# Performance work log

Hardware: AMD Instinct MI355X
Metric: run time of the kernel (lower is better)

## Reference

```python
import jax, jax.numpy as jnp
import numpy as np

N = 100000
E = 1600000
D_IN = 64
D_HID = 64


def setup_inputs() -> dict:
    key = jax.random.key(0)
    k1, k2, k3 = jax.random.split(key, 3)
    x = jax.random.normal(k1, (N, D_IN), dtype=jnp.float32)
    edge_index = jax.random.randint(k2, (2, E), 0, N, dtype=jnp.int64)
    # GCNConv linear weight (Glorot-like scale) and bias (zeros at init)
    W = jax.random.normal(k3, (D_IN, D_HID), dtype=jnp.float32) * (1.0 / np.sqrt(D_IN))
    b = jnp.zeros((D_HID,), dtype=jnp.float32)
    return {"x": x, "edge_index": edge_index, "W": W, "b": b}


def gcn_conv(x, edge_index, W, b):
    n = x.shape[0]
    # dense projection first (PyG GCNConv applies lin before propagate)
    xw = x @ W  # [N, D_HID]
    # add self-loops
    loop = jnp.arange(n, dtype=edge_index.dtype)
    src = jnp.concatenate([edge_index[0], loop])  # [E + N]
    dst = jnp.concatenate([edge_index[1], loop])
    # symmetric degree normalization with self-loops, unit edge weights
    ones = jnp.ones(src.shape[0], dtype=xw.dtype)
    deg = jax.ops.segment_sum(ones, dst, num_segments=n)  # [N]
    dinv = jnp.where(deg > 0, jax.lax.rsqrt(deg), 0.0)
    norm = dinv[src] * dinv[dst]  # [E + N]
    # gather, scale, scatter-add
    msgs = xw[src] * norm[:, None]  # [E + N, D_HID]
    out = jax.ops.segment_sum(msgs, dst, num_segments=n)  # [N, D_HID]
    return out + b


def reference(x, edge_index, W, b):
    return gcn_conv(x, edge_index, W, b)
```

## Files before the change

kernel.cpp:

```cpp
#include <hip/hip_runtime.h>
#include <hip/hip_fp16.h>

#define NN 100000
#define NE 1600000
#define D 64
#define SPAN 512
#define NB 196
#define BCAP 10240
#define ECH 4096
#define NP1 ((NE + ECH - 1) / ECH)
#define RB 128
#define NXB ((NN + RB - 1) / RB)
#define GN 64
#define GCAP 2048
#define NGB ((NN + GN - 1) / GN)

__global__ void __launch_bounds__(256)
k_part(const int* __restrict__ src, const int* __restrict__ dst,
       int* __restrict__ bcur, unsigned* __restrict__ brecs, int e) {
    __shared__ int hist[256];
    __shared__ int excl[256];
    __shared__ int cur[256];
    __shared__ int gbase[256];
    __shared__ int wsum[4];
    __shared__ unsigned stage[ECH];
    __shared__ unsigned char stgb[ECH];

    int tid  = threadIdx.x;
    int lane = tid & 63;
    int w    = tid >> 6;
    int e0   = blockIdx.x * ECH;
    int ecnt = min(ECH, e - e0);

    hist[tid] = 0;
    __syncthreads();

    unsigned rec[16];
    int      bk[16];
#pragma unroll
    for (int r = 0; r < 4; ++r) {
        int i = tid * 4 + r * 1024;
        if (i + 3 < ecnt) {
            int4 d = *(const int4*)(dst + e0 + i);
            int4 s = *(const int4*)(src + e0 + i);
            bk[r*4+0] = d.x >> 9; rec[r*4+0] = ((unsigned)s.x << 9) | (unsigned)(d.x & 511);
            bk[r*4+1] = d.y >> 9; rec[r*4+1] = ((unsigned)s.y << 9) | (unsigned)(d.y & 511);
            bk[r*4+2] = d.z >> 9; rec[r*4+2] = ((unsigned)s.z << 9) | (unsigned)(d.z & 511);
            bk[r*4+3] = d.w >> 9; rec[r*4+3] = ((unsigned)s.w << 9) | (unsigned)(d.w & 511);
            atomicAdd(&hist[bk[r*4+0]], 1);
            atomicAdd(&hist[bk[r*4+1]], 1);
            atomicAdd(&hist[bk[r*4+2]], 1);
            atomicAdd(&hist[bk[r*4+3]], 1);
        } else {
#pragma unroll
            for (int j = 0; j < 4; ++j) {
                int idx = i + j;
                if (idx < ecnt) {
                    int dd = dst[e0 + idx], ss = src[e0 + idx];
                    bk[r*4+j] = dd >> 9;
                    rec[r*4+j] = ((unsigned)ss << 9) | (unsigned)(dd & 511);
                    atomicAdd(&hist[bk[r*4+j]], 1);
                } else {
                    bk[r*4+j] = -1;
                }
            }
        }
    }
    __syncthreads();

    int v = hist[tid];
    int inc = v;
#pragma unroll
    for (int off = 1; off < 64; off <<= 1) {
        int t = __shfl_up(inc, off, 64);
        if (lane >= off) inc += t;
    }
    if (lane == 63) wsum[w] = inc;
    __syncthreads();
    int wo = 0;
#pragma unroll
    for (int j = 0; j < 4; ++j) wo += (j < w) ? wsum[j] : 0;
    int ex = wo + inc - v;
    excl[tid] = ex;
    cur[tid]  = ex;
    if (v > 0) gbase[tid] = atomicAdd(&bcur[tid], v);
    __syncthreads();

#pragma unroll
    for (int j = 0; j < 16; ++j) {
        if (bk[j] >= 0) {
            int p = atomicAdd(&cur[bk[j]], 1);
            stage[p] = rec[j];
            stgb[p]  = (unsigned char)bk[j];
        }
    }
    __syncthreads();

    for (int i = tid; i < ecnt; i += 256) {
        unsigned rc = stage[i];
        int bb = stgb[i];
        int gp = gbase[bb] + (i - excl[bb]);
        if (gp < BCAP)
            brecs[(size_t)bb * BCAP + gp] = rc;
    }
}

__global__ void __launch_bounds__(512)
k_fine(const unsigned* __restrict__ brecs, const int* __restrict__ bcur,
       int* __restrict__ cnt, int* __restrict__ rowstart,
       int* __restrict__ recs2, int n) {
    __shared__ int lcnt[SPAN];
    __shared__ int lcur[SPAN];
    __shared__ int wsum[8];
    __shared__ int sh_bbase;

    int b    = blockIdx.x;
    int tid  = threadIdx.x;
    int lane = tid & 63;
    int w    = tid >> 6;

    lcnt[tid] = 0;

    int bv = (tid < NB) ? min(bcur[tid], BCAP) : 0;
    int inc = bv;
#pragma unroll
    for (int off = 1; off < 64; off <<= 1) {
        int t = __shfl_up(inc, off, 64);
        if (lane >= off) inc += t;
    }
    if (lane == 63) wsum[w] = inc;
    __syncthreads();
    int wo = 0;
#pragma unroll
    for (int j = 0; j < 8; ++j) wo += (j < w) ? wsum[j] : 0;
    if (tid == b) sh_bbase = wo + inc - bv;

    int nrec = min(bcur[b], BCAP);
    const unsigned* rb = brecs + (size_t)b * BCAP;

    for (int i = tid; i < nrec; i += 512)
        atomicAdd(&lcnt[rb[i] & 511], 1);
    __syncthreads();

    int v = lcnt[tid];
    inc = v;
#pragma unroll
    for (int off = 1; off < 64; off <<= 1) {
        int t = __shfl_up(inc, off, 64);
        if (lane >= off) inc += t;
    }
    if (lane == 63) wsum[w] = inc;
    __syncthreads();
    wo = 0;
#pragma unroll
    for (int j = 0; j < 8; ++j) wo += (j < w) ? wsum[j] : 0;
    int ex = wo + inc - v;
    lcur[tid] = ex;

    int base = sh_bbase;
    int node = b * SPAN + tid;
    if (node < n) {
        cnt[node] = v;
        rowstart[node] = base + ex;
    }
    __syncthreads();

    for (int i = tid; i < nrec; i += 512) {
        unsigned rc = rb[i];
        int dl = rc & 511;
        int p = atomicAdd(&lcur[dl], 1);
        recs2[base + p] = (int)(rc >> 9);
    }
}

__global__ void __launch_bounds__(256, 3)
k_xw2h(const float* __restrict__ x, const float* __restrict__ W,
       const int* __restrict__ cnt, __half* __restrict__ xw2, int n) {
    __shared__ float sW[D][64];
    __shared__ float sx[RB][64];

    int tid = threadIdx.x;
    int wv  = tid >> 6;
    int l   = tid & 63;
    int rg  = l >> 3;
    int cg  = l & 7;
    int rowbase = blockIdx.x * RB;

#pragma unroll
    for (int i = 0; i < 4; ++i) {
        int f = i * 256 + tid;
        int k = f >> 4, c4 = (f & 15) * 4;
        *(float4*)(&sW[k][c4]) = *(const float4*)(W + k * D + c4);
    }
#pragma unroll
    for (int i = 0; i < 8; ++i) {
        int f = i * 256 + tid;
        int row = f >> 4, kc = f & 15;
        int gr = rowbase + row; if (gr >= n) gr = n - 1;
        float4 v = *(const float4*)(x + (size_t)gr * D + kc * 4);
        int sc = kc ^ ((row >> 3) & 7);
        *(float4*)(&sx[row][sc * 4]) = v;
    }
    __syncthreads();

    int rb0 = wv * 32 + rg * 4;
    float acc[4][8];
#pragma unroll
    for (int rr = 0; rr < 4; ++rr)
#pragma unroll
        for (int cc = 0; cc < 8; ++cc) acc[rr][cc] = 0.f;

    int swz = (rb0 >> 3) & 7;
    for (int ks = 0; ks < 16; ++ks) {
        float4 xv[4];
#pragma unroll
        for (int rr = 0; rr < 4; ++rr)
            xv[rr] = *(const float4*)(&sx[rb0 + rr][(ks ^ swz) * 4]);
#pragma unroll
        for (int j = 0; j < 4; ++j) {
            int k = ks * 4 + j;
            float4 w0 = *(const float4*)(&sW[k][cg * 8]);
            float4 w1 = *(const float4*)(&sW[k][cg * 8 + 4]);
#pragma unroll
            for (int rr = 0; rr < 4; ++rr) {
                float xs = (j == 0) ? xv[rr].x : (j == 1) ? xv[rr].y : (j == 2) ? xv[rr].z : xv[rr].w;
                acc[rr][0] += xs * w0.x;
                acc[rr][1] += xs * w0.y;
                acc[rr][2] += xs * w0.z;
                acc[rr][3] += xs * w0.w;
                acc[rr][4] += xs * w1.x;
                acc[rr][5] += xs * w1.y;
                acc[rr][6] += xs * w1.z;
                acc[rr][7] += xs * w1.w;
            }
        }
    }

    union H2U { __half2 h; unsigned u; };
#pragma unroll
    for (int rr = 0; rr < 4; ++rr) {
        int grow = rowbase + rb0 + rr;
        if (grow >= n) break;
        float di = rsqrtf((float)cnt[grow] + 1.0f);
        int4 pk;
        H2U a, bb, c, d;
        a.h  = __half2(__float2half_rn(acc[rr][0] * di), __float2half_rn(acc[rr][1] * di));
        bb.h = __half2(__float2half_rn(acc[rr][2] * di), __float2half_rn(acc[rr][3] * di));
        c.h  = __half2(__float2half_rn(acc[rr][4] * di), __float2half_rn(acc[rr][5] * di));
        d.h  = __half2(__float2half_rn(acc[rr][6] * di), __float2half_rn(acc[rr][7] * di));
        pk.x = (int)a.u; pk.y = (int)bb.u; pk.z = (int)c.u; pk.w = (int)d.u;
        *(int4*)(xw2 + (size_t)grow * D + cg * 8) = pk;
    }
}

__global__ void __launch_bounds__(256)
k_gather(const int* __restrict__ recs, const int* __restrict__ rowstart,
         const int* __restrict__ cnt, const __half* __restrict__ xw2,
         const float* __restrict__ b, float* __restrict__ out, int n) {
    __shared__ int lrs[GN];
    __shared__ int lcn[GN];
    __shared__ int lrec[GCAP];
    __shared__ int sh_tot;

    int tid = threadIdx.x;
    int n0  = blockIdx.x * GN;
    int nn  = min(GN, n - n0);

    if (tid < nn) {
        lrs[tid] = rowstart[n0 + tid];
        lcn[tid] = cnt[n0 + tid];
    }
    __syncthreads();
    if (tid == 0) sh_tot = lrs[nn - 1] + lcn[nn - 1] - lrs[0];
    __syncthreads();

    int bb  = lrs[0];
    int tot = sh_tot;
    for (int i = tid; i < tot && i < GCAP; i += 256)
        lrec[i] = recs[bb + i];
    __syncthreads();

    int w    = tid >> 6;
    int lane = tid & 63;
    int eg   = lane >> 3;
    int cb   = lane & 7;

    for (int nl = w; nl < nn; nl += 4) {
        int base_l = lrs[nl] - bb;
        int k      = lcn[nl];

        float acc[8];
#pragma unroll
        for (int j = 0; j < 8; ++j) acc[j] = 0.f;

        for (int i0 = 0; i0 < k; i0 += 16) {
            int e1 = i0 + eg;
            int e2 = i0 + 8 + eg;
            int4 v1 = make_int4(0, 0, 0, 0);
            int4 v2 = make_int4(0, 0, 0, 0);
            if (e1 < k) {
                int idx = base_l + e1;
                int s = (idx < GCAP) ? lrec[idx] : recs[bb + idx];
                v1 = *((const int4*)(xw2 + (size_t)s * D) + cb);
            }
            if (e2 < k) {
                int idx = base_l + e2;
                int s = (idx < GCAP) ? lrec[idx] : recs[bb + idx];
                v2 = *((const int4*)(xw2 + (size_t)s * D) + cb);
            }
            const __half2* h1 = (const __half2*)&v1;
            const __half2* h2 = (const __half2*)&v2;
#pragma unroll
            for (int j = 0; j < 4; ++j) {
                float2 f1 = __half22float2(h1[j]);
                float2 f2 = __half22float2(h2[j]);
                acc[2 * j]     += f1.x + f2.x;
                acc[2 * j + 1] += f1.y + f2.y;
            }
        }

#pragma unroll
        for (int m = 8; m < 64; m <<= 1)
#pragma unroll
            for (int j = 0; j < 8; ++j)
                acc[j] += __shfl_xor(acc[j], m, 64);

        if (eg == 0) {
            int node = n0 + nl;
            float di = rsqrtf((float)k + 1.0f);
            int4 sv = *((const int4*)(xw2 + (size_t)node * D) + cb);
            const __half2* sp = (const __half2*)&sv;
            float2 s0 = __half22float2(sp[0]);
            float2 s1 = __half22float2(sp[1]);
            float2 s2 = __half22float2(sp[2]);
            float2 s3 = __half22float2(sp[3]);
            float4 b0 = *(const float4*)(b + cb * 8);
            float4 b1 = *(const float4*)(b + cb * 8 + 4);
            float4 o0, o1;
            o0.x = (acc[0] + s0.x) * di + b0.x;
            o0.y = (acc[1] + s0.y) * di + b0.y;
            o0.z = (acc[2] + s1.x) * di + b0.z;
            o0.w = (acc[3] + s1.y) * di + b0.w;
            o1.x = (acc[4] + s2.x) * di + b1.x;
            o1.y = (acc[5] + s2.y) * di + b1.y;
            o1.z = (acc[6] + s3.x) * di + b1.z;
            o1.w = (acc[7] + s3.y) * di + b1.w;
            *(float4*)(out + (size_t)node * D + cb * 8)     = o0;
            *(float4*)(out + (size_t)node * D + cb * 8 + 4) = o1;
        }
    }
}

extern "C" void kernel_launch(void* const* d_in, const int* in_sizes, int n_in,
                              void* d_out, int out_size, void* d_ws, size_t ws_size,
                              hipStream_t stream) {
    const float* x  = (const float*)d_in[0];
    const int*   ei = (const int*)d_in[1];
    const float* W  = (const float*)d_in[2];
    const float* b  = (const float*)d_in[3];
    float* out = (float*)d_out;

    __half*   xw2      = (__half*)d_ws;
    int*      cnt      = (int*)(xw2 + (size_t)NN * D);
    int*      rowstart = cnt + NN;
    int*      bcur     = rowstart + NN;
    unsigned* brecs    = (unsigned*)(bcur + NB);
    int*      recs2    = (int*)(brecs + (size_t)NB * BCAP);

    const int* src = ei;
    const int* dst = ei + NE;

    hipMemsetAsync(bcur, 0, NB * sizeof(int), stream);

    k_part <<<NP1, 256, 0, stream>>>(src, dst, bcur, brecs, NE);
    k_fine <<<NB, 512, 0, stream>>>(brecs, bcur, cnt, rowstart, recs2, NN);
    k_xw2h <<<NXB, 256, 0, stream>>>(x, W, cnt, xw2, NN);

    k_gather<<<NGB, 256, 0, stream>>>(recs2, rowstart, cnt, xw2, b, out, NN);
}
```

Measured before the change: 102.6 us.

## Fuse fine bucket sort into gather kernel and compute degrees via global atomics

```diff
diff --git a/kernel.cpp b/kernel.cpp
--- a/kernel.cpp
+++ b/kernel.cpp
@@ -11,13 +11,11 @@
 #define NP1 ((NE + ECH - 1) / ECH)
 #define RB 128
 #define NXB ((NN + RB - 1) / RB)
-#define GN 64
-#define GCAP 2048
-#define NGB ((NN + GN - 1) / GN)
 
 __global__ void __launch_bounds__(256)
 k_part(const int* __restrict__ src, const int* __restrict__ dst,
-       int* __restrict__ bcur, unsigned* __restrict__ brecs, int e) {
+       int* __restrict__ cnt, int* __restrict__ bcur,
+       unsigned* __restrict__ brecs, int e) {
     __shared__ int hist[256];
     __shared__ int excl[256];
     __shared__ int cur[256];
@@ -51,6 +49,10 @@
             atomicAdd(&hist[bk[r*4+1]], 1);
             atomicAdd(&hist[bk[r*4+2]], 1);
             atomicAdd(&hist[bk[r*4+3]], 1);
+            atomicAdd(&cnt[d.x], 1);
+            atomicAdd(&cnt[d.y], 1);
+            atomicAdd(&cnt[d.z], 1);
+            atomicAdd(&cnt[d.w], 1);
         } else {
 #pragma unroll
             for (int j = 0; j < 4; ++j) {
@@ -60,6 +62,7 @@
                     bk[r*4+j] = dd >> 9;
                     rec[r*4+j] = ((unsigned)ss << 9) | (unsigned)(dd & 511);
                     atomicAdd(&hist[bk[r*4+j]], 1);
+                    atomicAdd(&cnt[dd], 1);
                 } else {
                     bk[r*4+j] = -1;
                 }
@@ -102,74 +105,6 @@
         int gp = gbase[bb] + (i - excl[bb]);
         if (gp < BCAP)
             brecs[(size_t)bb * BCAP + gp] = rc;
-    }
-}
-
-__global__ void __launch_bounds__(512)
-k_fine(const unsigned* __restrict__ brecs, const int* __restrict__ bcur,
-       int* __restrict__ cnt, int* __restrict__ rowstart,
-       int* __restrict__ recs2, int n) {
-    __shared__ int lcnt[SPAN];
-    __shared__ int lcur[SPAN];
-    __shared__ int wsum[8];
-    __shared__ int sh_bbase;
-
-    int b    = blockIdx.x;
-    int tid  = threadIdx.x;
-    int lane = tid & 63;
-    int w    = tid >> 6;
-
-    lcnt[tid] = 0;
-
-    int bv = (tid < NB) ? min(bcur[tid], BCAP) : 0;
-    int inc = bv;
-#pragma unroll
-    for (int off = 1; off < 64; off <<= 1) {
-        int t = __shfl_up(inc, off, 64);
-        if (lane >= off) inc += t;
-    }
-    if (lane == 63) wsum[w] = inc;
-    __syncthreads();
-    int wo = 0;
-#pragma unroll
-    for (int j = 0; j < 8; ++j) wo += (j < w) ? wsum[j] : 0;
-    if (tid == b) sh_bbase = wo + inc - bv;
-
-    int nrec = min(bcur[b], BCAP);
-    const unsigned* rb = brecs + (size_t)b * BCAP;
-
-    for (int i = tid; i < nrec; i += 512)
-        atomicAdd(&lcnt[rb[i] & 511], 1);
-    __syncthreads();
-
-    int v = lcnt[tid];
-    inc = v;
-#pragma unroll
-    for (int off = 1; off < 64; off <<= 1) {
-        int t = __shfl_up(inc, off, 64);
-        if (lane >= off) inc += t;
-    }
-    if (lane == 63) wsum[w] = inc;
-    __syncthreads();
-    wo = 0;
-#pragma unroll
-    for (int j = 0; j < 8; ++j) wo += (j < w) ? wsum[j] : 0;
-    int ex = wo + inc - v;
-    lcur[tid] = ex;
-
-    int base = sh_bbase;
-    int node = b * SPAN + tid;
-    if (node < n) {
-        cnt[node] = v;
-        rowstart[node] = base + ex;
-    }
-    __syncthreads();
-
-    for (int i = tid; i < nrec; i += 512) {
-        unsigned rc = rb[i];
-        int dl = rc & 511;
-        int p = atomicAdd(&lcur[dl], 1);
-        recs2[base + p] = (int)(rc >> 9);
     }
 }
 
@@ -253,41 +188,67 @@
     }
 }
 
-__global__ void __launch_bounds__(256)
-k_gather(const int* __restrict__ recs, const int* __restrict__ rowstart,
-         const int* __restrict__ cnt, const __half* __restrict__ xw2,
-         const float* __restrict__ b, float* __restrict__ out, int n) {
-    __shared__ int lrs[GN];
-    __shared__ int lcn[GN];
-    __shared__ int lrec[GCAP];
-    __shared__ int sh_tot;
-
-    int tid = threadIdx.x;
-    int n0  = blockIdx.x * GN;
-    int nn  = min(GN, n - n0);
-
-    if (tid < nn) {
-        lrs[tid] = rowstart[n0 + tid];
-        lcn[tid] = cnt[n0 + tid];
-    }
-    __syncthreads();
-    if (tid == 0) sh_tot = lrs[nn - 1] + lcn[nn - 1] - lrs[0];
-    __syncthreads();
-
-    int bb  = lrs[0];
-    int tot = sh_tot;
-    for (int i = tid; i < tot && i < GCAP; i += 256)
-        lrec[i] = recs[bb + i];
-    __syncthreads();
-
-    int w    = tid >> 6;
+__global__ void __launch_bounds__(1024)
+k_gfuse(const unsigned* __restrict__ brecs, const int* __restrict__ bcur,
+        const __half* __restrict__ xw2, const float* __restrict__ bias,
+        float* __restrict__ out) {
+    __shared__ int sorted[BCAP];
+    __shared__ int lcnt[SPAN];
+    __shared__ int lexcl[SPAN];
+    __shared__ int lcur[SPAN];
+    __shared__ int wsum[8];
+
+    int b    = blockIdx.x;
+    int tid  = threadIdx.x;
     int lane = tid & 63;
-    int eg   = lane >> 3;
-    int cb   = lane & 7;
-
-    for (int nl = w; nl < nn; nl += 4) {
-        int base_l = lrs[nl] - bb;
-        int k      = lcn[nl];
+    int wv   = tid >> 6;
+
+    if (tid < SPAN) lcnt[tid] = 0;
+    __syncthreads();
+
+    int nrec = min(bcur[b], BCAP);
+    const unsigned* rb = brecs + (size_t)b * BCAP;
+
+    for (int i = tid; i < nrec; i += 1024)
+        atomicAdd(&lcnt[rb[i] & 511], 1);
+    __syncthreads();
+
+    int v = 0, inc = 0;
+    if (tid < SPAN) {
+        v = lcnt[tid];
+        inc = v;
+#pragma unroll
+        for (int off = 1; off < 64; off <<= 1) {
+            int t = __shfl_up(inc, off, 64);
+            if (lane >= off) inc += t;
+        }
+        if (lane == 63) wsum[wv] = inc;
+    }
+    __syncthreads();
+    if (tid < SPAN) {
+        int wo = 0;
+#pragma unroll
+        for (int j = 0; j < 8; ++j) wo += (j < wv) ? wsum[j] : 0;
+        int ex = wo + inc - v;
+        lexcl[tid] = ex;
+        lcur[tid]  = ex;
+    }
+    __syncthreads();
+
+    for (int i = tid; i < nrec; i += 1024) {
+        unsigned r = rb[i];
+        sorted[atomicAdd(&lcur[r & 511], 1)] = (int)(r >> 9);
+    }
+    __syncthreads();
+
+    int eg = lane >> 3;
+    int cb = lane & 7;
+    int n0 = b * SPAN;
+    int nnode = min(SPAN, NN - n0);
+
+    for (int nl = wv; nl < nnode; nl += 16) {
+        int base_l = lexcl[nl];
+        int k      = lcnt[nl];
 
         float acc[8];
 #pragma unroll
@@ -299,13 +260,11 @@
             int4 v1 = make_int4(0, 0, 0, 0);
             int4 v2 = make_int4(0, 0, 0, 0);
             if (e1 < k) {
-                int idx = base_l + e1;
-                int s = (idx < GCAP) ? lrec[idx] : recs[bb + idx];
+                int s = sorted[base_l + e1];
                 v1 = *((const int4*)(xw2 + (size_t)s * D) + cb);
             }
             if (e2 < k) {
-                int idx = base_l + e2;
-                int s = (idx < GCAP) ? lrec[idx] : recs[bb + idx];
+                int s = sorted[base_l + e2];
                 v2 = *((const int4*)(xw2 + (size_t)s * D) + cb);
             }
             const __half2* h1 = (const __half2*)&v1;
@@ -334,8 +293,8 @@
             float2 s1 = __half22float2(sp[1]);
             float2 s2 = __half22float2(sp[2]);
             float2 s3 = __half22float2(sp[3]);
-            float4 b0 = *(const float4*)(b + cb * 8);
-            float4 b1 = *(const float4*)(b + cb * 8 + 4);
+            float4 b0 = *(const float4*)(bias + cb * 8);
+            float4 b1 = *(const float4*)(bias + cb * 8 + 4);
             float4 o0, o1;
             o0.x = (acc[0] + s0.x) * di + b0.x;
             o0.y = (acc[1] + s0.y) * di + b0.y;
@@ -360,21 +319,17 @@
     const float* b  = (const float*)d_in[3];
     float* out = (float*)d_out;
 
-    __half*   xw2      = (__half*)d_ws;
-    int*      cnt      = (int*)(xw2 + (size_t)NN * D);
-    int*      rowstart = cnt + NN;
-    int*      bcur     = rowstart + NN;
-    unsigned* brecs    = (unsigned*)(bcur + NB);
-    int*      recs2    = (int*)(brecs + (size_t)NB * BCAP);
+    __half*   xw2   = (__half*)d_ws;
+    int*      cnt   = (int*)(xw2 + (size_t)NN * D);
+    int*      bcur  = cnt + NN;
+    unsigned* brecs = (unsigned*)(bcur + NB);
 
     const int* src = ei;
     const int* dst = ei + NE;
 
-    hipMemsetAsync(bcur, 0, NB * sizeof(int), stream);
-
-    k_part <<<NP1, 256, 0, stream>>>(src, dst, bcur, brecs, NE);
-    k_fine <<<NB, 512, 0, stream>>>(brecs, bcur, cnt, rowstart, recs2, NN);
+    hipMemsetAsync(cnt, 0, (size_t)(NN + NB) * sizeof(int), stream);
+
+    k_part <<<NP1, 256, 0, stream>>>(src, dst, cnt, bcur, brecs, NE);
     k_xw2h <<<NXB, 256, 0, stream>>>(x, W, cnt, xw2, NN);
-
-    k_gather<<<NGB, 256, 0, stream>>>(recs2, rowstart, cnt, xw2, b, out, NN);
+    k_gfuse<<<NB, 1024, 0, stream>>>(brecs, bcur, xw2, b, out);
 }
```

Result: slower. 157.7 us (+53.8%).

## Split projected features into column-octant slices and gather per octant

Applied to the files above, without the earlier changes.

```diff
diff --git a/kernel.cpp b/kernel.cpp
--- a/kernel.cpp
+++ b/kernel.cpp
@@ -13,7 +13,8 @@
 #define NXB ((NN + RB - 1) / RB)
 #define GN 64
 #define GCAP 2048
-#define NGB ((NN + GN - 1) / GN)
+#define NGRP ((NN + GN - 1) / GN)
+#define NOCT 8
 
 __global__ void __launch_bounds__(256)
 k_part(const int* __restrict__ src, const int* __restrict__ dst,
@@ -175,7 +176,7 @@
 
 __global__ void __launch_bounds__(256, 3)
 k_xw2h(const float* __restrict__ x, const float* __restrict__ W,
-       const int* __restrict__ cnt, __half* __restrict__ xw2, int n) {
+       const int* __restrict__ cnt, int4* __restrict__ xwc, int n) {
     __shared__ float sW[D][64];
     __shared__ float sx[RB][64];
 
@@ -249,26 +250,28 @@
         c.h  = __half2(__float2half_rn(acc[rr][4] * di), __float2half_rn(acc[rr][5] * di));
         d.h  = __half2(__float2half_rn(acc[rr][6] * di), __float2half_rn(acc[rr][7] * di));
         pk.x = (int)a.u; pk.y = (int)bb.u; pk.z = (int)c.u; pk.w = (int)d.u;
-        *(int4*)(xw2 + (size_t)grow * D + cg * 8) = pk;
+        xwc[(size_t)cg * NN + grow] = pk;
     }
 }
 
 __global__ void __launch_bounds__(256)
-k_gather(const int* __restrict__ recs, const int* __restrict__ rowstart,
-         const int* __restrict__ cnt, const __half* __restrict__ xw2,
-         const float* __restrict__ b, float* __restrict__ out, int n) {
+k_gather2(const int* __restrict__ recs, const int* __restrict__ rowstart,
+          const int* __restrict__ cnt, const int4* __restrict__ xwc,
+          const float* __restrict__ bias, float* __restrict__ out, int n) {
     __shared__ int lrs[GN];
     __shared__ int lcn[GN];
     __shared__ int lrec[GCAP];
     __shared__ int sh_tot;
 
+    int oct = blockIdx.x & 7;
+    int g   = blockIdx.x >> 3;
     int tid = threadIdx.x;
-    int n0  = blockIdx.x * GN;
+    int n0  = g * GN;
     int nn  = min(GN, n - n0);
 
     if (tid < nn) {
-        lrs[tid] = rowstart[n0 + tid];
-        lcn[tid] = cnt[n0 + tid];
+        lrs[tid] = __builtin_nontemporal_load(rowstart + n0 + tid);
+        lcn[tid] = __builtin_nontemporal_load(cnt + n0 + tid);
     }
     __syncthreads();
     if (tid == 0) sh_tot = lrs[nn - 1] + lcn[nn - 1] - lrs[0];
@@ -277,65 +280,59 @@
     int bb  = lrs[0];
     int tot = sh_tot;
     for (int i = tid; i < tot && i < GCAP; i += 256)
-        lrec[i] = recs[bb + i];
-    __syncthreads();
-
-    int w    = tid >> 6;
+        lrec[i] = __builtin_nontemporal_load(recs + bb + i);
+    __syncthreads();
+
+    const int4* slice = xwc + (size_t)oct * NN;
+
+    int wv   = tid >> 6;
     int lane = tid & 63;
-    int eg   = lane >> 3;
-    int cb   = lane & 7;
-
-    for (int nl = w; nl < nn; nl += 4) {
-        int base_l = lrs[nl] - bb;
-        int k      = lcn[nl];
+    int sub  = lane >> 4;
+    int es   = lane & 15;
+
+    for (int p = wv * 4; p < nn; p += 16) {
+        int nl = p + sub;
+        bool live = (nl < nn);
+        int base_l = live ? (lrs[nl] - bb) : 0;
+        int k      = live ? lcn[nl] : 0;
 
         float acc[8];
 #pragma unroll
         for (int j = 0; j < 8; ++j) acc[j] = 0.f;
 
         for (int i0 = 0; i0 < k; i0 += 16) {
-            int e1 = i0 + eg;
-            int e2 = i0 + 8 + eg;
-            int4 v1 = make_int4(0, 0, 0, 0);
-            int4 v2 = make_int4(0, 0, 0, 0);
-            if (e1 < k) {
-                int idx = base_l + e1;
+            int e = i0 + es;
+            if (e < k) {
+                int idx = base_l + e;
                 int s = (idx < GCAP) ? lrec[idx] : recs[bb + idx];
-                v1 = *((const int4*)(xw2 + (size_t)s * D) + cb);
+                int4 v = slice[s];
+                const __half2* hp = (const __half2*)&v;
+#pragma unroll
+                for (int j = 0; j < 4; ++j) {
+                    float2 f = __half22float2(hp[j]);
+                    acc[2 * j]     += f.x;
+                    acc[2 * j + 1] += f.y;
+                }
             }
-            if (e2 < k) {
-                int idx = base_l + e2;
-                int s = (idx < GCAP) ? lrec[idx] : recs[bb + idx];
-                v2 = *((const int4*)(xw2 + (size_t)s * D) + cb);
-            }
-            const __half2* h1 = (const __half2*)&v1;
-            const __half2* h2 = (const __half2*)&v2;
-#pragma unroll
-            for (int j = 0; j < 4; ++j) {
-                float2 f1 = __half22float2(h1[j]);
-                float2 f2 = __half22float2(h2[j]);
-                acc[2 * j]     += f1.x + f2.x;
-                acc[2 * j + 1] += f1.y + f2.y;
-            }
-        }
-
-#pragma unroll
-        for (int m = 8; m < 64; m <<= 1)
+        }
+
+#pragma unroll
+        for (int m = 1; m < 16; m <<= 1)
 #pragma unroll
             for (int j = 0; j < 8; ++j)
                 acc[j] += __shfl_xor(acc[j], m, 64);
 
-        if (eg == 0) {
+        if (es == 0 && live) {
             int node = n0 + nl;
             float di = rsqrtf((float)k + 1.0f);
-            int4 sv = *((const int4*)(xw2 + (size_t)node * D) + cb);
+            int4 sv = slice[node];
             const __half2* sp = (const __half2*)&sv;
             float2 s0 = __half22float2(sp[0]);
             float2 s1 = __half22float2(sp[1]);
             float2 s2 = __half22float2(sp[2]);
             float2 s3 = __half22float2(sp[3]);
-            float4 b0 = *(const float4*)(b + cb * 8);
-            float4 b1 = *(const float4*)(b + cb * 8 + 4);
+            float4 b0 = *(const float4*)(bias + oct * 8);
+            float4 b1 = *(const float4*)(bias + oct * 8 + 4);
             float4 o0, o1;
             o0.x = (acc[0] + s0.x) * di + b0.x;
             o0.y = (acc[1] + s0.y) * di + b0.y;
@@ -345,8 +342,8 @@
             o1.y = (acc[5] + s2.y) * di + b1.y;
             o1.z = (acc[6] + s3.x) * di + b1.z;
             o1.w = (acc[7] + s3.y) * di + b1.w;
-            *(float4*)(out + (size_t)node * D + cb * 8)     = o0;
-            *(float4*)(out + (size_t)node * D + cb * 8 + 4) = o1;
+            *(float4*)(out + (size_t)node * D + oct * 8)     = o0;
+            *(float4*)(out + (size_t)node * D + oct * 8 + 4) = o1;
         }
     }
 }
@@ -360,8 +357,8 @@
     const float* b  = (const float*)d_in[3];
     float* out = (float*)d_out;
 
-    __half*   xw2      = (__half*)d_ws;
-    int*      cnt      = (int*)(xw2 + (size_t)NN * D);
+    int4*     xwc      = (int4*)d_ws;
+    int*      cnt      = (int*)(xwc + (size_t)NOCT * NN);
     int*      rowstart = cnt + NN;
     int*      bcur     = rowstart + NN;
     unsigned* brecs    = (unsigned*)(bcur + NB);
@@ -372,9 +369,8 @@
 
     hipMemsetAsync(bcur, 0, NB * sizeof(int), stream);
 
-    k_part <<<NP1, 256, 0, stream>>>(src, dst, bcur, brecs, NE);
-    k_fine <<<NB, 512, 0, stream>>>(brecs, bcur, cnt, rowstart, recs2, NN);
-    k_xw2h <<<NXB, 256, 0, stream>>>(x, W, cnt, xw2, NN);
-
-    k_gather<<<NGB, 256, 0, stream>>>(recs2, rowstart, cnt, xw2, b, out, NN);
-}
+    k_part   <<<NP1, 256, 0, stream>>>(src, dst, bcur, brecs, NE);
+    k_fine   <<<NB, 512, 0, stream>>>(brecs, bcur, cnt, rowstart, recs2, NN);
+    k_xw2h   <<<NXB, 256, 0, stream>>>(x, W, cnt, xwc, NN);
+    k_gather2<<<NGRP * 8, 256, 0, stream>>>(recs2, rowstart, cnt, xwc, b, out, NN);
+}
```

Result: slower. 175.0 us (+70.6%).
